# Performance work log

Measured on AMD Instinct MI355X. Metric: run time of the kernel, lower is better.

Reference implementation:

```python
import jax, jax.numpy as jnp
import numpy as np

NEG_SLOPE = 0.2
EPS = 1e-16  # PyG softmax denominator epsilon


def gatv2_layer(x, src, dst, W_l, W_r, att, bias, num_nodes, heads, out_dim, concat):
    # x: [N, F_in]; src/dst: [E] (self-loops already included)
    x_l = (x @ W_l).reshape(num_nodes, heads, out_dim)  # source transform
    x_r = (x @ W_r).reshape(num_nodes, heads, out_dim)  # target transform
    # GATv2 scoring: a^T LeakyReLU(x_l[j] + x_r[i])
    e = jax.nn.leaky_relu(x_l[src] + x_r[dst], NEG_SLOPE)       # [E, H, D]
    logits = jnp.einsum('ehd,hd->eh', e, att)                    # [E, H]
    # segment softmax over incoming edges of each target node
    m = jax.ops.segment_max(logits, dst, num_segments=num_nodes)  # [N, H]
    ex = jnp.exp(logits - m[dst])                                 # [E, H]
    denom = jax.ops.segment_sum(ex, dst, num_segments=num_nodes)  # [N, H]
    alpha = ex / (denom[dst] + EPS)                               # [E, H]
    msg = x_l[src] * alpha[:, :, None]                            # [E, H, D]
    out = jax.ops.segment_sum(msg, dst, num_segments=num_nodes)   # [N, H, D]
    if concat:
        out = out.reshape(num_nodes, heads * out_dim)
    else:
        out = out.mean(axis=1)
    return out + bias


def setup_inputs() -> dict:
    key = jax.random.key(0)
    ks = jax.random.split(key, 10)
    N, E, F_in, H, D, F_out = 50000, 400000, 256, 4, 128, 64

    def glorot(k, shape, fan):
        return jax.random.normal(k, shape, dtype=jnp.float32) * (1.0 / np.sqrt(fan))

    return {
        'x': jax.random.normal(ks[0], (N, F_in), dtype=jnp.float32),
        'edge_index': jax.random.randint(ks[1], (2, E), 0, N, dtype=jnp.int64),
        'W_l1': glorot(ks[2], (F_in, H * D), F_in),
        'W_r1': glorot(ks[3], (F_in, H * D), F_in),
        'att1': glorot(ks[4], (H, D), D),
        'b1': jnp.zeros((H * D,), dtype=jnp.float32),
        'W_l2': glorot(ks[5], (H * D, F_out), H * D),
        'W_r2': glorot(ks[6], (H * D, F_out), H * D),
        'att2': glorot(ks[7], (1, F_out), F_out),
        'b2': jnp.zeros((F_out,), dtype=jnp.float32),
    }


def reference(x, edge_index, W_l1, W_r1, att1, b1, W_l2, W_r2, att2, b2):
    N = x.shape[0]
    # add self-loops (PyG GATv2Conv default add_self_loops=True)
    loops = jnp.arange(N, dtype=edge_index.dtype)
    src = jnp.concatenate([edge_index[0], loops])
    dst = jnp.concatenate([edge_index[1], loops])
    # dropout(p=0.6) is identity in eval mode
    h = gatv2_layer(x, src, dst, W_l1, W_r1, att1, b1, N, heads=4, out_dim=128, concat=True)
    h = jax.nn.elu(h)
    out = gatv2_layer(h, src, dst, W_l2, W_r2, att2, b2, N, heads=1, out_dim=64, concat=False)
    return out
```

## Files before the change

kernel.cpp:

```cpp
#include <hip/hip_runtime.h>
#include <hip/hip_bf16.h>
#include <math.h>


#define NEG_SLOPE 0.2f

typedef _Float16 half8 __attribute__((ext_vector_type(8)));
typedef _Float16 h2 __attribute__((ext_vector_type(2)));
typedef float f32x4 __attribute__((ext_vector_type(4)));


__global__ __launch_bounds__(256) void k_count(const int* __restrict__ ei, int* __restrict__ counts,
                                               int E, int Etot) {
    int i = blockIdx.x * 256 + threadIdx.x;
    if (i >= Etot) return;
    int dst = (i < E) ? ei[E + i] : (i - E);
    atomicAdd(&counts[dst], 1);
}

__global__ __launch_bounds__(1024) void k_scan_a(const int* __restrict__ counts, int* __restrict__ offs,
                                                 int* __restrict__ partial, int n) {
    __shared__ int buf[1024];
    int b = blockIdx.x, t = threadIdx.x;
    int i = b * 1024 + t;
    int v = (i < n) ? counts[i] : 0;
    buf[t] = v;
    __syncthreads();
    #pragma unroll
    for (int off = 1; off < 1024; off <<= 1) {
        int add = (t >= off) ? buf[t - off] : 0;
        __syncthreads();
        buf[t] += add;
        __syncthreads();
    }
    if (i < n) offs[i + 1] = buf[t];
    if (t == 1023) partial[b] = buf[1023];
}

__global__ __launch_bounds__(1024) void k_scan_b(int* __restrict__ partial, int nb) {
    __shared__ int buf[1024];
    int t = threadIdx.x;
    int v = (t < nb) ? partial[t] : 0;
    buf[t] = v;
    __syncthreads();
    #pragma unroll
    for (int off = 1; off < 1024; off <<= 1) {
        int add = (t >= off) ? buf[t - off] : 0;
        __syncthreads();
        buf[t] += add;
        __syncthreads();
    }
    if (t < nb) partial[t] = buf[t] - v;
}

__global__ __launch_bounds__(256) void k_scan_c(int* __restrict__ offs, int* __restrict__ cursor,
                                                const int* __restrict__ partial, int n) {
    int i = blockIdx.x * 256 + threadIdx.x;
    if (i == 0) { offs[0] = 0; cursor[0] = 0; }
    if (i < n) {
        int v = offs[i + 1] + partial[i >> 10];
        offs[i + 1] = v;
        cursor[i + 1] = v;
    }
}

__global__ __launch_bounds__(256) void k_fill(const int* __restrict__ ei, int* __restrict__ cursor,
                                              int* __restrict__ csr_src, int E, int Etot) {
    int i = blockIdx.x * 256 + threadIdx.x;
    if (i >= Etot) return;
    int src, dst;
    if (i < E) { src = ei[i]; dst = ei[E + i]; }
    else       { src = i - E; dst = i - E; }
    int pos = atomicAdd(&cursor[dst], 1);
    csr_src[pos] = src;
}


__global__ __launch_bounds__(256) void k_cast_x(const float* __restrict__ in, _Float16* __restrict__ out,
                                                int n8) {
    int i = blockIdx.x * 256 + threadIdx.x;
    if (i >= n8) return;
    const float4* p = (const float4*)(in + i * 8);
    float4 a = p[0], b = p[1];
    half8 v;
    v[0] = (_Float16)a.x; v[1] = (_Float16)a.y; v[2] = (_Float16)a.z; v[3] = (_Float16)a.w;
    v[4] = (_Float16)b.x; v[5] = (_Float16)b.y; v[6] = (_Float16)b.z; v[7] = (_Float16)b.w;
    *(half8*)(out + i * 8) = v;
}

__global__ __launch_bounds__(256) void k_cast_w(const float* __restrict__ Wl1, const float* __restrict__ Wr1,
                                                const float* __restrict__ Wl2, const float* __restrict__ Wr2,
                                                _Float16* __restrict__ W1T, _Float16* __restrict__ W2T) {
    int i = blockIdx.x * 256 + threadIdx.x;
    const int T1 = 1024 * 256;
    const int T2 = 128 * 512;
    if (i < T1) {
        int n = i >> 8, k = i & 255;
        float v = (n < 512) ? Wl1[k * 512 + n] : Wr1[k * 512 + (n - 512)];
        W1T[i] = (_Float16)v;
    } else if (i < T1 + T2) {
        int j = i - T1;
        int n = j >> 9, k = j & 511;
        float v = (n < 64) ? Wl2[k * 64 + n] : Wr2[k * 64 + (n - 64)];
        W2T[j] = (_Float16)v;
    }
}


#define LDSPITCH 40

__global__ __launch_bounds__(256) void k_gemm_f16(const _Float16* __restrict__ A,
                                                  const _Float16* __restrict__ Bt,
                                                  _Float16* __restrict__ C,
                                                  int M, int N, int K, int ntiles) {
    __shared__ _Float16 As[128 * LDSPITCH];
    __shared__ _Float16 Bs[128 * LDSPITCH];

    int tid = threadIdx.x;
    int lane = tid & 63;
    int wave = tid >> 6;
    int wm = wave >> 1, wn = wave & 1;
    int l15 = lane & 15, q = lane >> 4;

    int ntile = blockIdx.x % ntiles;
    int mtile = blockIdx.x / ntiles;
    int tileM = mtile * 128;
    int tileN = ntile * 128;

    int srow = tid >> 2;
    int scg  = (tid & 3) * 8;

    f32x4 acc[4][4];
    #pragma unroll
    for (int i = 0; i < 4; ++i)
        #pragma unroll
        for (int j = 0; j < 4; ++j)
            acc[i][j] = (f32x4)(0.f);

    for (int k0 = 0; k0 < K; k0 += 32) {
        float4 va0, va1, vb0, vb1;
        {
            int r0 = tileM + srow, r1 = tileM + srow + 64;
            const float4 z = make_float4(0.f, 0.f, 0.f, 0.f);
            va0 = (r0 < M) ? *(const float4*)(A + (long)r0 * K + k0 + scg) : z;
            va1 = (r1 < M) ? *(const float4*)(A + (long)r1 * K + k0 + scg) : z;
            vb0 = *(const float4*)(Bt + (long)(tileN + srow) * K + k0 + scg);
            vb1 = *(const float4*)(Bt + (long)(tileN + srow + 64) * K + k0 + scg);
        }
        __syncthreads();
        *(float4*)(As + srow * LDSPITCH + scg) = va0;
        *(float4*)(As + (srow + 64) * LDSPITCH + scg) = va1;
        *(float4*)(Bs + srow * LDSPITCH + scg) = vb0;
        *(float4*)(Bs + (srow + 64) * LDSPITCH + scg) = vb1;
        __syncthreads();

        half8 af[4], bf[4];
        #pragma unroll
        for (int i = 0; i < 4; ++i)
            af[i] = *(half8*)(As + (wm * 64 + i * 16 + l15) * LDSPITCH + q * 8);
        #pragma unroll
        for (int j = 0; j < 4; ++j)
            bf[j] = *(half8*)(Bs + (wn * 64 + j * 16 + l15) * LDSPITCH + q * 8);
        #pragma unroll
        for (int i = 0; i < 4; ++i)
            #pragma unroll
            for (int j = 0; j < 4; ++j)
                acc[i][j] = __builtin_amdgcn_mfma_f32_16x16x32_f16(af[i], bf[j], acc[i][j], 0, 0, 0);
    }

    #pragma unroll
    for (int i = 0; i < 4; ++i) {
        #pragma unroll
        for (int r = 0; r < 4; ++r) {
            int grow = tileM + wm * 64 + i * 16 + q * 4 + r;
            if (grow < M) {
                #pragma unroll
                for (int j = 0; j < 4; ++j) {
                    int gcol = tileN + wn * 64 + j * 16 + l15;
                    C[(long)grow * N + gcol] = (_Float16)acc[i][j][r];
                }
            }
        }
    }
}


__device__ __forceinline__ float dot2acc(h2 a, h2 b, float c) {
#if __has_builtin(__builtin_amdgcn_fdot2)
    return __builtin_amdgcn_fdot2(a, b, c, false);
#else
    return fmaf((float)a[1], (float)b[1], fmaf((float)a[0], (float)b[0], c));
#endif
}

__global__ __launch_bounds__(256) void k_attn1(const _Float16* __restrict__ xlr,
                                               const float* __restrict__ att, const float* __restrict__ b1,
                                               const int* __restrict__ offs, const int* __restrict__ csr_src,
                                               _Float16* __restrict__ hout, int N) {
    int wave = threadIdx.x >> 6;
    int lane = threadIdx.x & 63;
    int node = blockIdx.x * 4 + wave;
    if (node >= N) return;

    int cbase = (lane >> 4) * 128 + (lane & 15) * 8;

    half8 xrv8 = *(const half8*)(xlr + (long)node * 1024 + 512 + cbase);
    h2 xr[4], at[4];
    #pragma unroll
    for (int j = 0; j < 4; ++j) {
        xr[j][0] = xrv8[2 * j]; xr[j][1] = xrv8[2 * j + 1];
        at[j][0] = (_Float16)att[cbase + 2 * j];
        at[j][1] = (_Float16)att[cbase + 2 * j + 1];
    }
    const h2 ns2 = {(_Float16)NEG_SLOPE, (_Float16)NEG_SLOPE};

    float l = 0.f;
    float acc[8] = {};

    int e0 = offs[node], e1 = offs[node + 1];
    int s_next = csr_src[e0];
    int s_next2 = (e0 + 1 < e1) ? csr_src[e0 + 1] : 0;
    half8 xlv = *(const half8*)(xlr + (long)s_next * 1024 + cbase);

    for (int e = e0; e < e1; ++e) {
        half8 cur = xlv;
        int s_pf = s_next2;
        if (e + 2 < e1) s_next2 = csr_src[e + 2];
        if (e + 1 < e1) xlv = *(const half8*)(xlr + (long)s_pf * 1024 + cbase);

        const h2* cp = (const h2*)&cur;
        float p = 0.f;
        #pragma unroll
        for (int j = 0; j < 4; ++j) {
            h2 t = cp[j] + xr[j];
#if __has_builtin(__builtin_elementwise_max)
            t = __builtin_elementwise_max(t, t * ns2);
#else
            h2 tn = t * ns2;
            t[0] = (t[0] > tn[0]) ? t[0] : tn[0];
            t[1] = (t[1] > tn[1]) ? t[1] : tn[1];
#endif
            p = dot2acc(t, at[j], p);
        }
        #pragma unroll
        for (int off = 1; off <= 8; off <<= 1) p += __shfl_xor(p, off, 64);
        float w = __expf(p);
        l += w;
        #pragma unroll
        for (int j = 0; j < 8; ++j) acc[j] = fmaf(w, (float)cur[j], acc[j]);
    }

    float inv = 1.f / (l + 1e-16f);
    half8 ov;
    #pragma unroll
    for (int j = 0; j < 8; ++j) {
        float o = fmaf(acc[j], inv, b1[cbase + j]);
        o = (o > 0.f) ? o : (__expf(o) - 1.f);
        ov[j] = (_Float16)o;
    }
    *(half8*)(hout + (long)node * 512 + cbase) = ov;
}


__global__ __launch_bounds__(256) void k_attn2(const _Float16* __restrict__ xlr2,
                                               const float* __restrict__ att, const float* __restrict__ b2,
                                               const int* __restrict__ offs, const int* __restrict__ csr_src,
                                               float* __restrict__ out, int N) {
    int wave = threadIdx.x >> 6;
    int lane = threadIdx.x & 63;
    int node = blockIdx.x * 4 + wave;
    if (node >= N) return;

    float xrv = (float)xlr2[(long)node * 128 + 64 + lane];
    float av  = att[lane];

    float l = 0.f, acc = 0.f;
    int e0 = offs[node], e1 = offs[node + 1];
    int s_next = csr_src[e0];
    int s_next2 = (e0 + 1 < e1) ? csr_src[e0 + 1] : 0;
    float xlv = (float)xlr2[(long)s_next * 128 + lane];

    for (int e = e0; e < e1; ++e) {
        float x = xlv;
        int s_pf = s_next2;
        if (e + 2 < e1) s_next2 = csr_src[e + 2];
        if (e + 1 < e1) xlv = (float)xlr2[(long)s_pf * 128 + lane];

        float t = x + xrv;
        t = fmaxf(t, NEG_SLOPE * t);
        float p = t * av;
        #pragma unroll
        for (int off = 1; off <= 32; off <<= 1) p += __shfl_xor(p, off, 64);
        float w = __expf(p);
        l += w;
        acc = fmaf(w, x, acc);
    }
    out[(long)node * 64 + lane] = acc / (l + 1e-16f) + b2[lane];
}


extern "C" void kernel_launch(void* const* d_in, const int* in_sizes, int n_in,
                              void* d_out, int out_size, void* d_ws, size_t ws_size,
                              hipStream_t stream) {
    const float* x    = (const float*)d_in[0];
    const int*   ei   = (const int*)d_in[1];
    const float* Wl1  = (const float*)d_in[2];
    const float* Wr1  = (const float*)d_in[3];
    const float* att1 = (const float*)d_in[4];
    const float* b1   = (const float*)d_in[5];
    const float* Wl2  = (const float*)d_in[6];
    const float* Wr2  = (const float*)d_in[7];
    const float* att2 = (const float*)d_in[8];
    const float* b2   = (const float*)d_in[9];
    float* out = (float*)d_out;

    const int F_IN = 256;
    int N = in_sizes[0] / F_IN;
    int E = in_sizes[1] / 2;
    int Etot = E + N;
    int nScanBlocks = (N + 1023) / 1024;

    char* p = (char*)d_ws;
    auto carve = [&](size_t bytes) -> void* {
        void* r = (void*)p;
        p += (bytes + 255) & ~(size_t)255;
        return r;
    };
    _Float16* xh   = (_Float16*)carve((size_t)N * 256 * 2);
    _Float16* W1T  = (_Float16*)carve((size_t)1024 * 256 * 2);
    _Float16* W2T  = (_Float16*)carve((size_t)128 * 512 * 2);
    _Float16* C1   = (_Float16*)carve((size_t)N * 1024 * 2);
    _Float16* h    = (_Float16*)carve((size_t)N * 512 * 2);
    _Float16* C2   = (_Float16*)carve((size_t)N * 128 * 2);
    int* counts  = (int*)carve((size_t)N * 4);
    int* offs    = (int*)carve((size_t)(N + 1) * 4);
    int* cursor  = (int*)carve((size_t)(N + 1) * 4);
    int* partial = (int*)carve((size_t)nScanBlocks * 4);
    int* csr     = (int*)carve((size_t)Etot * 4);

    int gN    = (N + 255) / 256;
    int gEtot = (Etot + 255) / 256;

    k_cast_x<<<(N * 256 / 8 + 255) / 256, 256, 0, stream>>>(x, xh, N * 256 / 8);
    {
        int total = 1024 * 256 + 128 * 512;
        k_cast_w<<<(total + 255) / 256, 256, 0, stream>>>(Wl1, Wr1, Wl2, Wr2, W1T, W2T);
    }

    hipMemsetAsync(counts, 0, (size_t)N * 4, stream);
    k_count<<<gEtot, 256, 0, stream>>>(ei, counts, E, Etot);
    k_scan_a<<<nScanBlocks, 1024, 0, stream>>>(counts, offs, partial, N);
    k_scan_b<<<1, 1024, 0, stream>>>(partial, nScanBlocks);
    k_scan_c<<<gN, 256, 0, stream>>>(offs, cursor, partial, N);
    k_fill<<<gEtot, 256, 0, stream>>>(ei, cursor, csr, E, Etot);

    {
        int mtiles = (N + 127) / 128, ntiles = 1024 / 128;
        k_gemm_f16<<<mtiles * ntiles, 256, 0, stream>>>(xh, W1T, C1, N, 1024, 256, ntiles);
    }
    k_attn1<<<(N + 3) / 4, 256, 0, stream>>>(C1, att1, b1, offs, csr, h, N);

    {
        int mtiles = (N + 127) / 128;
        k_gemm_f16<<<mtiles, 256, 0, stream>>>(h, W2T, C2, N, 128, 512, 1);
    }
    k_attn2<<<(N + 3) / 4, 256, 0, stream>>>(C2, att2, b2, offs, csr, out, N);
}
```

Measured before the change: 372.8 us.

## Fuse setup kernels, use direct global-to-LDS GEMM loads, split edges across half-waves

Merges the x cast with edge counting and the weight cast with the first scan pass into shared launches, which cuts launch count. The GEMM now loads tiles straight into LDS through global_load_lds into an XOR-swizzled unpadded layout, dropping the row bounds checks by padding the workspace. Both attention kernels process two edges at once, one per half-wave, and combine the partial sums with a cross-half shuffle, giving more memory parallelism per wave. The padded rows of xh and h are never written, so the GEMM reads uninitialised workspace; only output rows below N are stored, so results for valid rows should be unaffected.

```diff
diff --git a/kernel.cpp b/kernel.cpp
--- a/kernel.cpp
+++ b/kernel.cpp
@@ -9,32 +9,84 @@
 typedef _Float16 h2 __attribute__((ext_vector_type(2)));
 typedef float f32x4 __attribute__((ext_vector_type(4)));
 
-
-__global__ __launch_bounds__(256) void k_count(const int* __restrict__ ei, int* __restrict__ counts,
-                                               int E, int Etot) {
-    int i = blockIdx.x * 256 + threadIdx.x;
-    if (i >= Etot) return;
-    int dst = (i < E) ? ei[E + i] : (i - E);
-    atomicAdd(&counts[dst], 1);
-}
-
-__global__ __launch_bounds__(1024) void k_scan_a(const int* __restrict__ counts, int* __restrict__ offs,
-                                                 int* __restrict__ partial, int n) {
+#if __has_builtin(__builtin_amdgcn_global_load_lds)
+#define HAS_GLL 1
+__device__ __forceinline__ void gll16(const _Float16* g, _Float16* l) {
+    __builtin_amdgcn_global_load_lds(
+        (const __attribute__((address_space(1))) unsigned int*)g,
+        (__attribute__((address_space(3))) unsigned int*)l, 16, 0, 0);
+}
+#endif
+
+__device__ __forceinline__ float dot2acc(h2 a, h2 b, float c) {
+#if __has_builtin(__builtin_amdgcn_fdot2)
+    return __builtin_amdgcn_fdot2(a, b, c, false);
+#else
+    return fmaf((float)a[1], (float)b[1], fmaf((float)a[0], (float)b[0], c));
+#endif
+}
+
+
+__global__ __launch_bounds__(256) void k_castx_count(const float* __restrict__ x, _Float16* __restrict__ xh,
+                                                     int n8, const int* __restrict__ ei,
+                                                     int* __restrict__ counts, int E, int Etot, int gEtot) {
+    int b = blockIdx.x;
+    if (b < gEtot) {
+        int i = b * 256 + threadIdx.x;
+        if (i < Etot) {
+            int dst = (i < E) ? ei[E + i] : (i - E);
+            atomicAdd(&counts[dst], 1);
+        }
+    } else {
+        int i = (b - gEtot) * 256 + threadIdx.x;
+        if (i < n8) {
+            const float4* p = (const float4*)(x + i * 8);
+            float4 a = p[0], c = p[1];
+            half8 v;
+            v[0] = (_Float16)a.x; v[1] = (_Float16)a.y; v[2] = (_Float16)a.z; v[3] = (_Float16)a.w;
+            v[4] = (_Float16)c.x; v[5] = (_Float16)c.y; v[6] = (_Float16)c.z; v[7] = (_Float16)c.w;
+            *(half8*)(xh + i * 8) = v;
+        }
+    }
+}
+
+
+__global__ __launch_bounds__(1024) void k_castw_scana(const int* __restrict__ counts, int* __restrict__ offs,
+                                                      int* __restrict__ partial, int n, int nsb,
+                                                      const float* __restrict__ Wl1, const float* __restrict__ Wr1,
+                                                      const float* __restrict__ Wl2, const float* __restrict__ Wr2,
+                                                      _Float16* __restrict__ W1T, _Float16* __restrict__ W2T) {
     __shared__ int buf[1024];
     int b = blockIdx.x, t = threadIdx.x;
-    int i = b * 1024 + t;
-    int v = (i < n) ? counts[i] : 0;
-    buf[t] = v;
-    __syncthreads();
-    #pragma unroll
-    for (int off = 1; off < 1024; off <<= 1) {
-        int add = (t >= off) ? buf[t - off] : 0;
+    if (b < nsb) {
+        int i = b * 1024 + t;
+        int v = (i < n) ? counts[i] : 0;
+        buf[t] = v;
         __syncthreads();
-        buf[t] += add;
-        __syncthreads();
-    }
-    if (i < n) offs[i + 1] = buf[t];
-    if (t == 1023) partial[b] = buf[1023];
+        #pragma unroll
+        for (int off = 1; off < 1024; off <<= 1) {
+            int add = (t >= off) ? buf[t - off] : 0;
+            __syncthreads();
+            buf[t] += add;
+            __syncthreads();
+        }
+        if (i < n) offs[i + 1] = buf[t];
+        if (t == 1023) partial[b] = buf[1023];
+    } else {
+        int i = (b - nsb) * 1024 + t;
+        const int T1 = 1024 * 256;
+        const int T2 = 128 * 512;
+        if (i < T1) {
+            int nn = i >> 8, k = i & 255;
+            float v = (nn < 512) ? Wl1[k * 512 + nn] : Wr1[k * 512 + (nn - 512)];
+            W1T[i] = (_Float16)v;
+        } else if (i < T1 + T2) {
+            int j = i - T1;
+            int nn = j >> 9, k = j & 511;
+            float v = (nn < 64) ? Wl2[k * 64 + nn] : Wr2[k * 64 + (nn - 64)];
+            W2T[j] = (_Float16)v;
+        }
+    }
 }
 
 __global__ __launch_bounds__(1024) void k_scan_b(int* __restrict__ partial, int nb) {
@@ -76,45 +128,12 @@
 }
 
 
-__global__ __launch_bounds__(256) void k_cast_x(const float* __restrict__ in, _Float16* __restrict__ out,
-                                                int n8) {
-    int i = blockIdx.x * 256 + threadIdx.x;
-    if (i >= n8) return;
-    const float4* p = (const float4*)(in + i * 8);
-    float4 a = p[0], b = p[1];
-    half8 v;
-    v[0] = (_Float16)a.x; v[1] = (_Float16)a.y; v[2] = (_Float16)a.z; v[3] = (_Float16)a.w;
-    v[4] = (_Float16)b.x; v[5] = (_Float16)b.y; v[6] = (_Float16)b.z; v[7] = (_Float16)b.w;
-    *(half8*)(out + i * 8) = v;
-}
-
-__global__ __launch_bounds__(256) void k_cast_w(const float* __restrict__ Wl1, const float* __restrict__ Wr1,
-                                                const float* __restrict__ Wl2, const float* __restrict__ Wr2,
-                                                _Float16* __restrict__ W1T, _Float16* __restrict__ W2T) {
-    int i = blockIdx.x * 256 + threadIdx.x;
-    const int T1 = 1024 * 256;
-    const int T2 = 128 * 512;
-    if (i < T1) {
-        int n = i >> 8, k = i & 255;
-        float v = (n < 512) ? Wl1[k * 512 + n] : Wr1[k * 512 + (n - 512)];
-        W1T[i] = (_Float16)v;
-    } else if (i < T1 + T2) {
-        int j = i - T1;
-        int n = j >> 9, k = j & 511;
-        float v = (n < 64) ? Wl2[k * 64 + n] : Wr2[k * 64 + (n - 64)];
-        W2T[j] = (_Float16)v;
-    }
-}
-
-
-#define LDSPITCH 40
-
 __global__ __launch_bounds__(256) void k_gemm_f16(const _Float16* __restrict__ A,
                                                   const _Float16* __restrict__ Bt,
                                                   _Float16* __restrict__ C,
                                                   int M, int N, int K, int ntiles) {
-    __shared__ _Float16 As[128 * LDSPITCH];
-    __shared__ _Float16 Bs[128 * LDSPITCH];
+    __shared__ _Float16 As[128 * 32];
+    __shared__ _Float16 Bs[128 * 32];
 
     int tid = threadIdx.x;
     int lane = tid & 63;
@@ -127,8 +146,18 @@
     int tileM = mtile * 128;
     int tileN = ntile * 128;
 
-    int srow = tid >> 2;
-    int scg  = (tid & 3) * 8;
+    int srow = lane >> 2;
+    int schunk = (lane & 3) ^ ((lane >> 3) & 3);
+    const _Float16* gA0 = A + (long)(tileM + wave * 32 + srow) * K + schunk * 8;
+    const _Float16* gA1 = gA0 + (long)16 * K;
+    const _Float16* gB0 = Bt + (long)(tileN + wave * 32 + srow) * K + schunk * 8;
+    const _Float16* gB1 = gB0 + (long)16 * K;
+    _Float16* lA0 = As + wave * 1024;
+    _Float16* lA1 = lA0 + 512;
+    _Float16* lB0 = Bs + wave * 1024;
+    _Float16* lB1 = lB0 + 512;
+
+    int aswz = (q ^ ((l15 >> 1) & 3)) * 8;
 
     f32x4 acc[4][4];
     #pragma unroll
@@ -138,34 +167,36 @@
             acc[i][j] = (f32x4)(0.f);
 
     for (int k0 = 0; k0 < K; k0 += 32) {
-        float4 va0, va1, vb0, vb1;
-        {
-            int r0 = tileM + srow, r1 = tileM + srow + 64;
-            const float4 z = make_float4(0.f, 0.f, 0.f, 0.f);
-            va0 = (r0 < M) ? *(const float4*)(A + (long)r0 * K + k0 + scg) : z;
-            va1 = (r1 < M) ? *(const float4*)(A + (long)r1 * K + k0 + scg) : z;
-            vb0 = *(const float4*)(Bt + (long)(tileN + srow) * K + k0 + scg);
-            vb1 = *(const float4*)(Bt + (long)(tileN + srow + 64) * K + k0 + scg);
-        }
+#ifdef HAS_GLL
+        gll16(gA0 + k0, lA0);
+        gll16(gA1 + k0, lA1);
+        gll16(gB0 + k0, lB0);
+        gll16(gB1 + k0, lB1);
+#else
+        half8 va0 = *(const half8*)(gA0 + k0);
+        half8 va1 = *(const half8*)(gA1 + k0);
+        half8 vb0 = *(const half8*)(gB0 + k0);
+        half8 vb1 = *(const half8*)(gB1 + k0);
+        *(half8*)(lA0 + lane * 8) = va0;
+        *(half8*)(lA1 + lane * 8) = va1;
+        *(half8*)(lB0 + lane * 8) = vb0;
+        *(half8*)(lB1 + lane * 8) = vb1;
+#endif
         __syncthreads();
-        *(float4*)(As + srow * LDSPITCH + scg) = va0;
-        *(float4*)(As + (srow + 64) * LDSPITCH + scg) = va1;
-        *(float4*)(Bs + srow * LDSPITCH + scg) = vb0;
-        *(float4*)(Bs + (srow + 64) * LDSPITCH + scg) = vb1;
-        __syncthreads();
 
         half8 af[4], bf[4];
         #pragma unroll
         for (int i = 0; i < 4; ++i)
-            af[i] = *(half8*)(As + (wm * 64 + i * 16 + l15) * LDSPITCH + q * 8);
+            af[i] = *(const half8*)(As + (wm * 64 + i * 16 + l15) * 32 + aswz);
         #pragma unroll
         for (int j = 0; j < 4; ++j)
-            bf[j] = *(half8*)(Bs + (wn * 64 + j * 16 + l15) * LDSPITCH + q * 8);
+            bf[j] = *(const half8*)(Bs + (wn * 64 + j * 16 + l15) * 32 + aswz);
         #pragma unroll
         for (int i = 0; i < 4; ++i)
             #pragma unroll
             for (int j = 0; j < 4; ++j)
                 acc[i][j] = __builtin_amdgcn_mfma_f32_16x16x32_f16(af[i], bf[j], acc[i][j], 0, 0, 0);
+        __syncthreads();
     }
 
     #pragma unroll
@@ -185,14 +216,6 @@
 }
 
 
-__device__ __forceinline__ float dot2acc(h2 a, h2 b, float c) {
-#if __has_builtin(__builtin_amdgcn_fdot2)
-    return __builtin_amdgcn_fdot2(a, b, c, false);
-#else
-    return fmaf((float)a[1], (float)b[1], fmaf((float)a[0], (float)b[0], c));
-#endif
-}
-
 __global__ __launch_bounds__(256) void k_attn1(const _Float16* __restrict__ xlr,
                                                const float* __restrict__ att, const float* __restrict__ b1,
                                                const int* __restrict__ offs, const int* __restrict__ csr_src,
@@ -202,37 +225,50 @@
     int node = blockIdx.x * 4 + wave;
     if (node >= N) return;
 
-    int cbase = (lane >> 4) * 128 + (lane & 15) * 8;
-
-    half8 xrv8 = *(const half8*)(xlr + (long)node * 1024 + 512 + cbase);
-    h2 xr[4], at[4];
+    int eh = lane >> 5;
+    int hl = lane & 31;
+    int cbase = (hl >> 3) * 128 + (hl & 7) * 16;
+
+    half8 xra = *(const half8*)(xlr + (long)node * 1024 + 512 + cbase);
+    half8 xrb = *(const half8*)(xlr + (long)node * 1024 + 512 + cbase + 8);
+    h2 xr[8], at[8];
     #pragma unroll
     for (int j = 0; j < 4; ++j) {
-        xr[j][0] = xrv8[2 * j]; xr[j][1] = xrv8[2 * j + 1];
+        xr[j][0] = xra[2 * j];     xr[j][1] = xra[2 * j + 1];
+        xr[4 + j][0] = xrb[2 * j]; xr[4 + j][1] = xrb[2 * j + 1];
+    }
+    #pragma unroll
+    for (int j = 0; j < 8; ++j) {
         at[j][0] = (_Float16)att[cbase + 2 * j];
         at[j][1] = (_Float16)att[cbase + 2 * j + 1];
     }
     const h2 ns2 = {(_Float16)NEG_SLOPE, (_Float16)NEG_SLOPE};
 
     float l = 0.f;
-    float acc[8] = {};
+    float acc[16] = {};
 
     int e0 = offs[node], e1 = offs[node + 1];
-    int s_next = csr_src[e0];
-    int s_next2 = (e0 + 1 < e1) ? csr_src[e0 + 1] : 0;
-    half8 xlv = *(const half8*)(xlr + (long)s_next * 1024 + cbase);
-
-    for (int e = e0; e < e1; ++e) {
-        half8 cur = xlv;
-        int s_pf = s_next2;
-        if (e + 2 < e1) s_next2 = csr_src[e + 2];
-        if (e + 1 < e1) xlv = *(const half8*)(xlr + (long)s_pf * 1024 + cbase);
-
-        const h2* cp = (const h2*)&cur;
+    int e = e0 + eh;
+    half8 c0, c1;
+    if (e < e1) {
+        int s = csr_src[e];
+        c0 = *(const half8*)(xlr + (long)s * 1024 + cbase);
+        c1 = *(const half8*)(xlr + (long)s * 1024 + cbase + 8);
+    }
+    while (e < e1) {
+        half8 u0 = c0, u1 = c1;
+        int en = e + 2;
+        if (en < e1) {
+            int s = csr_src[en];
+            c0 = *(const half8*)(xlr + (long)s * 1024 + cbase);
+            c1 = *(const half8*)(xlr + (long)s * 1024 + cbase + 8);
+        }
+        const h2* up = (const h2*)&u0;
+        const h2* vp = (const h2*)&u1;
         float p = 0.f;
         #pragma unroll
         for (int j = 0; j < 4; ++j) {
-            h2 t = cp[j] + xr[j];
+            h2 t = up[j] + xr[j];
 #if __has_builtin(__builtin_elementwise_max)
             t = __builtin_elementwise_max(t, t * ns2);
 #else
@@ -243,22 +279,51 @@
             p = dot2acc(t, at[j], p);
         }
         #pragma unroll
-        for (int off = 1; off <= 8; off <<= 1) p += __shfl_xor(p, off, 64);
+        for (int j = 0; j < 4; ++j) {
+            h2 t = vp[j] + xr[4 + j];
+#if __has_builtin(__builtin_elementwise_max)
+            t = __builtin_elementwise_max(t, t * ns2);
+#else
+            h2 tn = t * ns2;
+            t[0] = (t[0] > tn[0]) ? t[0] : tn[0];
+            t[1] = (t[1] > tn[1]) ? t[1] : tn[1];
+#endif
+            p = dot2acc(t, at[4 + j], p);
+        }
+        p += __shfl_xor(p, 1, 64);
+        p += __shfl_xor(p, 2, 64);
+        p += __shfl_xor(p, 4, 64);
         float w = __expf(p);
         l += w;
         #pragma unroll
-        for (int j = 0; j < 8; ++j) acc[j] = fmaf(w, (float)cur[j], acc[j]);
-    }
-
-    float inv = 1.f / (l + 1e-16f);
-    half8 ov;
-    #pragma unroll
-    for (int j = 0; j < 8; ++j) {
-        float o = fmaf(acc[j], inv, b1[cbase + j]);
-        o = (o > 0.f) ? o : (__expf(o) - 1.f);
-        ov[j] = (_Float16)o;
-    }
-    *(half8*)(hout + (long)node * 512 + cbase) = ov;
+        for (int j = 0; j < 8; ++j) acc[j] = fmaf(w, (float)u0[j], acc[j]);
+        #pragma unroll
+        for (int j = 0; j < 8; ++j) acc[8 + j] = fmaf(w, (float)u1[j], acc[8 + j]);
+        e = en;
+    }
+
+    l += __shfl_xor(l, 32, 64);
+    #pragma unroll
+    for (int j = 0; j < 16; ++j) acc[j] += __shfl_xor(acc[j], 32, 64);
+
+    if (eh == 0) {
+        float inv = 1.f / (l + 1e-16f);
+        half8 o0, o1;
+        #pragma unroll
+        for (int j = 0; j < 8; ++j) {
+            float o = fmaf(acc[j], inv, b1[cbase + j]);
+            o = (o > 0.f) ? o : (__expf(o) - 1.f);
+            o0[j] = (_Float16)o;
+        }
+        #pragma unroll
+        for (int j = 0; j < 8; ++j) {
+            float o = fmaf(acc[8 + j], inv, b1[cbase + 8 + j]);
+            o = (o > 0.f) ? o : (__expf(o) - 1.f);
+            o1[j] = (_Float16)o;
+        }
+        *(half8*)(hout + (long)node * 512 + cbase) = o0;
+        *(half8*)(hout + (long)node * 512 + cbase + 8) = o1;
+    }
 }
 
 
@@ -271,31 +336,59 @@
     int node = blockIdx.x * 4 + wave;
     if (node >= N) return;
 
-    float xrv = (float)xlr2[(long)node * 128 + 64 + lane];
-    float av  = att[lane];
-
-    float l = 0.f, acc = 0.f;
+    int eh = lane >> 5;
+    int hl = lane & 31;
+    int ch = hl * 2;
+
+    h2 xrh = *(const h2*)(xlr2 + (long)node * 128 + 64 + ch);
+    h2 ath; ath[0] = (_Float16)att[ch]; ath[1] = (_Float16)att[ch + 1];
+    const h2 ns2 = {(_Float16)NEG_SLOPE, (_Float16)NEG_SLOPE};
+
+    float l = 0.f, a0 = 0.f, a1 = 0.f;
     int e0 = offs[node], e1 = offs[node + 1];
-    int s_next = csr_src[e0];
-    int s_next2 = (e0 + 1 < e1) ? csr_src[e0 + 1] : 0;
-    float xlv = (float)xlr2[(long)s_next * 128 + lane];
-
-    for (int e = e0; e < e1; ++e) {
-        float x = xlv;
-        int s_pf = s_next2;
-        if (e + 2 < e1) s_next2 = csr_src[e + 2];
-        if (e + 1 < e1) xlv = (float)xlr2[(long)s_pf * 128 + lane];
-
-        float t = x + xrv;
-        t = fmaxf(t, NEG_SLOPE * t);
-        float p = t * av;
-        #pragma unroll
-        for (int off = 1; off <= 32; off <<= 1) p += __shfl_xor(p, off, 64);
+    int e = e0 + eh;
+    h2 cv;
+    if (e < e1) {
+        int s = csr_src[e];
+        cv = *(const h2*)(xlr2 + (long)s * 128 + ch);
+    }
+    while (e < e1) {
+        h2 u = cv;
+        int en = e + 2;
+        if (en < e1) {
+            int s = csr_src[en];
+            cv = *(const h2*)(xlr2 + (long)s * 128 + ch);
+        }
+        h2 t = u + xrh;
+#if __has_builtin(__builtin_elementwise_max)
+        t = __builtin_elementwise_max(t, t * ns2);
+#else
+        h2 tn = t * ns2;
+        t[0] = (t[0] > tn[0]) ? t[0] : tn[0];
+        t[1] = (t[1] > tn[1]) ? t[1] : tn[1];
+#endif
+        float p = dot2acc(t, ath, 0.f);
+        p += __shfl_xor(p, 1, 64);
+        p += __shfl_xor(p, 2, 64);
+        p += __shfl_xor(p, 4, 64);
+        p += __shfl_xor(p, 8, 64);
+        p += __shfl_xor(p, 16, 64);
         float w = __expf(p);
         l += w;
-        acc = fmaf(w, x, acc);
-    }
-    out[(long)node * 64 + lane] = acc / (l + 1e-16f) + b2[lane];
+        a0 = fmaf(w, (float)u[0], a0);
+        a1 = fmaf(w, (float)u[1], a1);
+        e = en;
+    }
+    l += __shfl_xor(l, 32, 64);
+    a0 += __shfl_xor(a0, 32, 64);
+    a1 += __shfl_xor(a1, 32, 64);
+    if (eh == 0) {
+        float inv = 1.f / (l + 1e-16f);
+        float2 o;
+        o.x = fmaf(a0, inv, b2[ch]);
+        o.y = fmaf(a1, inv, b2[ch + 1]);
+        *(float2*)(out + (long)node * 64 + ch) = o;
+    }
 }
 
 
@@ -319,6 +412,8 @@
     int E = in_sizes[1] / 2;
     int Etot = E + N;
     int nScanBlocks = (N + 1023) / 1024;
+    int mtiles = (N + 127) / 128;
+    int Mpad = mtiles * 128;
 
     char* p = (char*)d_ws;
     auto carve = [&](size_t bytes) -> void* {
@@ -326,11 +421,11 @@
         p += (bytes + 255) & ~(size_t)255;
         return r;
     };
-    _Float16* xh   = (_Float16*)carve((size_t)N * 256 * 2);
+    _Float16* xh   = (_Float16*)carve((size_t)Mpad * 256 * 2);
     _Float16* W1T  = (_Float16*)carve((size_t)1024 * 256 * 2);
     _Float16* W2T  = (_Float16*)carve((size_t)128 * 512 * 2);
     _Float16* C1   = (_Float16*)carve((size_t)N * 1024 * 2);
-    _Float16* h    = (_Float16*)carve((size_t)N * 512 * 2);
+    _Float16* h    = (_Float16*)carve((size_t)Mpad * 512 * 2);
     _Float16* C2   = (_Float16*)carve((size_t)N * 128 * 2);
     int* counts  = (int*)carve((size_t)N * 4);
     int* offs    = (int*)carve((size_t)(N + 1) * 4);
@@ -340,29 +435,26 @@
 
     int gN    = (N + 255) / 256;
     int gEtot = (Etot + 255) / 256;
-
-    k_cast_x<<<(N * 256 / 8 + 255) / 256, 256, 0, stream>>>(x, xh, N * 256 / 8);
+    int n8    = N * 256 / 8;
+    int gCast = (n8 + 255) / 256;
+
+    hipMemsetAsync(counts, 0, (size_t)N * 4, stream);
+
+    k_castx_count<<<gEtot + gCast, 256, 0, stream>>>(x, xh, n8, ei, counts, E, Etot, gEtot);
+
     {
         int total = 1024 * 256 + 128 * 512;
-        k_cast_w<<<(total + 255) / 256, 256, 0, stream>>>(Wl1, Wr1, Wl2, Wr2, W1T, W2T);
-    }
-
-    hipMemsetAsync(counts, 0, (size_t)N * 4, stream);
-    k_count<<<gEtot, 256, 0, stream>>>(ei, counts, E, Etot);
-    k_scan_a<<<nScanBlocks, 1024, 0, stream>>>(counts, offs, partial, N);
+        int gW = (total + 1023) / 1024;
+        k_castw_scana<<<nScanBlocks + gW, 1024, 0, stream>>>(counts, offs, partial, N, nScanBlocks,
+                                                             Wl1, Wr1, Wl2, Wr2, W1T, W2T);
+    }
     k_scan_b<<<1, 1024, 0, stream>>>(partial, nScanBlocks);
     k_scan_c<<<gN, 256, 0, stream>>>(offs, cursor, partial, N);
     k_fill<<<gEtot, 256, 0, stream>>>(ei, cursor, csr, E, Etot);
 
-    {
-        int mtiles = (N + 127) / 128, ntiles = 1024 / 128;
-        k_gemm_f16<<<mtiles * ntiles, 256, 0, stream>>>(xh, W1T, C1, N, 1024, 256, ntiles);
-    }
+    k_gemm_f16<<<mtiles * 8, 256, 0, stream>>>(xh, W1T, C1, N, 1024, 256, 8);
     k_attn1<<<(N + 3) / 4, 256, 0, stream>>>(C1, att1, b1, offs, csr, h, N);
 
-    {
-        int mtiles = (N + 127) / 128;
-        k_gemm_f16<<<mtiles, 256, 0, stream>>>(h, W2T, C2, N, 128, 512, 1);
-    }
+    k_gemm_f16<<<mtiles, 256, 0, stream>>>(h, W2T, C2, N, 128, 512, 1);
     k_attn2<<<(N + 3) / 4, 256, 0, stream>>>(C2, att2, b2, offs, csr, out, N);
 }
```

Result: faster. 348.1 us (-6.6%).
